# Kernel tuning notes

Measured on AMD Instinct MI355X. Metric: run time of the kernel, lower is better.

The kernel has to match this reference:

```python
import jax, jax.numpy as jnp
import numpy as np

WIN = (7, 7)
SHIFT = (3, 3)
HEADS = 8


def _rel_index():
    coords = np.stack(np.meshgrid(np.arange(WIN[0]), np.arange(WIN[1]), indexing='ij')).reshape(2, -1)
    rel = (coords[:, :, None] - coords[:, None, :]).transpose(1, 2, 0)  # [N,N,2]
    rel[:, :, 0] += WIN[0] - 1
    rel[:, :, 1] += WIN[1] - 1
    rel[:, :, 0] *= 2 * WIN[1] - 1
    return jnp.asarray(rel.sum(-1).reshape(-1).astype(np.int32))  # [N*N]


def _attn_mask(pad_H, pad_W):
    # standard Swin shifted-window mask (intended behavior of the source's mask block)
    img = np.zeros((pad_H, pad_W), np.float32)
    cnt = 0
    for h in ((0, -WIN[0]), (-WIN[0], -SHIFT[0]), (-SHIFT[0], None)):
        for w in ((0, -WIN[1]), (-WIN[1], -SHIFT[1]), (-SHIFT[1], None)):
            img[h[0]:h[1], w[0]:w[1]] = cnt
            cnt += 1
    nHw, nWw = pad_H // WIN[0], pad_W // WIN[1]
    m = img.reshape(nHw, WIN[0], nWw, WIN[1]).transpose(0, 2, 1, 3).reshape(nHw * nWw, WIN[0] * WIN[1])
    diff = m[:, None, :] - m[:, :, None]  # [nW, N, N]
    return jnp.asarray(np.where(diff != 0, -100.0, 0.0).astype(np.float32))


def setup_inputs() -> dict:
    key = jax.random.key(0)
    ks = jax.random.split(key, 6)
    B, H, W, C = 32, 56, 56, 256
    return {
        'x': jax.random.normal(ks[0], (B, H, W, C), jnp.float32),
        'qkv_weight': jax.random.normal(ks[1], (3 * C, C), jnp.float32) * (C ** -0.5),
        'qkv_bias': jnp.zeros((3 * C,), jnp.float32),
        'proj_weight': jax.random.normal(ks[2], (C, C), jnp.float32) * (C ** -0.5),
        'proj_bias': jnp.zeros((C,), jnp.float32),
        'rel_bias_table': jax.random.normal(ks[3], ((2 * WIN[0] - 1) * (2 * WIN[1] - 1), HEADS), jnp.float32) * 0.02,
        'rel_index': _rel_index(),
    }


def reference(x, qkv_weight, qkv_bias, proj_weight, proj_bias, rel_bias_table, rel_index):
    B, H, W, C = x.shape
    hd = C // HEADS
    N = WIN[0] * WIN[1]
    # relative position bias: [1, heads, N, N]
    bias = rel_bias_table[rel_index].reshape(N, N, HEADS).transpose(2, 0, 1)[None]
    # H, W chosen divisible by window -> pad is a no-op; cyclic shift
    xs = jnp.roll(x, (-SHIFT[0], -SHIFT[1]), axis=(1, 2))
    nHw, nWw = H // WIN[0], W // WIN[1]
    nW = nHw * nWw
    xw = xs.reshape(B, nHw, WIN[0], nWw, WIN[1], C).transpose(0, 1, 3, 2, 4, 5).reshape(B * nW, N, C)
    qkv = xw @ qkv_weight.T + qkv_bias                           # [B*nW, N, 3C]
    qkv = qkv.reshape(B * nW, N, 3, HEADS, hd).transpose(2, 0, 3, 1, 4)
    q, k, v = qkv[0] * hd ** -0.5, qkv[1], qkv[2]                # [B*nW, heads, N, hd]
    attn = jnp.einsum('whnd,whmd->whnm', q, k) + bias            # [B*nW, heads, N, N]
    mask = _attn_mask(H, W)                                      # [nW, N, N]
    attn = attn.reshape(B, nW, HEADS, N, N) + mask[None, :, None]
    attn = jax.nn.softmax(attn, axis=-1).reshape(B * nW, HEADS, N, N)
    out = jnp.einsum('whnm,whmd->wnhd', attn, v).reshape(B * nW, N, C)
    out = out @ proj_weight.T + proj_bias
    out = out.reshape(B, nHw, nWw, WIN[0], WIN[1], C).transpose(0, 1, 3, 2, 4, 5).reshape(B, H, W, C)
    out = jnp.roll(out, (SHIFT[0], SHIFT[1]), axis=(1, 2))
    return out
```

## Files before the change

### kernel.cpp

```cpp
#include <hip/hip_runtime.h>

typedef float f32x4 __attribute__((ext_vector_type(4)));
typedef __bf16 bf16x4 __attribute__((ext_vector_type(4)));
typedef __bf16 bf16x8 __attribute__((ext_vector_type(8)));
typedef short s16x4 __attribute__((ext_vector_type(4)));

#define DEVI static __device__ __forceinline__

DEVI f32x4 mfma_k32(bf16x8 a, bf16x8 b, f32x4 c) {
    return __builtin_amdgcn_mfma_f32_16x16x32_bf16(a, b, c, 0, 0, 0);
}

union B4 { bf16x4 h; s16x4 s; };
DEVI f32x4 mfma_k16(bf16x4 a, bf16x4 b, f32x4 c) {
    B4 ua, ub; ua.h = a; ub.h = b;
    return __builtin_amdgcn_mfma_f32_16x16x16bf16_1k(ua.s, ub.s, c, 0, 0, 0);
}

union F8 { bf16x8 v; bf16x4 h[2]; };

DEVI bf16x8 ld8_lds(const __bf16* p) {
    F8 f;
    f.h[0] = *(const bf16x4*)p;
    f.h[1] = *(const bf16x4*)(p + 4);
    return f.v;
}
DEVI bf16x8 ld8_gb(const __bf16* p) { return *(const bf16x8*)p; }
DEVI bf16x8 ldf8(const float* p) {
    f32x4 a = *(const f32x4*)p;
    f32x4 b = *(const f32x4*)(p + 4);
    F8 f;
#pragma unroll
    for (int j = 0; j < 4; ++j) {
        f.h[0][j] = (__bf16)a[j];
        f.h[1][j] = (__bf16)b[j];
    }
    return f.v;
}

__global__ __launch_bounds__(256) void k_w2bf(const float* __restrict__ wqkv,
                                              const float* __restrict__ wp,
                                              __bf16* __restrict__ o) {
    int i = blockIdx.x * 256 + threadIdx.x;
    int t = i >> 9, kc = (i >> 6) & 7, l = i & 63;
    int row = t * 16 + (l & 15);
    int col = kc * 32 + (l >> 4) * 8;
    const float* src = (t < 48) ? (wqkv + row * 256 + col)
                                : (wp + (row - 768) * 256 + col);
    f32x4 a = *(const f32x4*)src;
    f32x4 b = *(const f32x4*)(src + 4);
    F8 f;
#pragma unroll
    for (int j = 0; j < 4; ++j) { f.h[0][j] = (__bf16)a[j]; f.h[1][j] = (__bf16)b[j]; }
    *(bf16x8*)(o + (size_t)i * 8) = f.v;
}

__global__ __launch_bounds__(512)
__attribute__((amdgpu_waves_per_eu(4))) void k_swin(
    const float* __restrict__ x,
    const __bf16* __restrict__ wb,
    const float* __restrict__ bqkv,
    const float* __restrict__ btab,
    const float* __restrict__ pbias,
    float* __restrict__ out)
{
    __shared__ __align__(16) unsigned char smem[53936];
    __bf16* xw = (__bf16*)(smem);
    __bf16* cb = (__bf16*)(smem + 25480);
    __bf16* tb = (__bf16*)(smem + 50960);
    unsigned* tinfo = (unsigned*)(smem + 53680);

    const int tid = threadIdx.x;
    const int wid = tid >> 6, lane = tid & 63;
    const int li = lane & 15, g = lane >> 4;
    const int blk = blockIdx.x;
    const int b = blk >> 6, wi = blk & 63;
    const int wh = wi >> 3, ww = wi & 7;
    const int h = wid;

    for (int c = tid; c < 49 * 32; c += 512) {
        int tok = c >> 5, part = c & 31;
        int i = tok / 7, j = tok - 7 * i;
        int r = wh * 7 + i + 3;  if (r >= 56) r -= 56;
        int cc = ww * 7 + j + 3; if (cc >= 56) cc -= 56;
        F8 f; f.v = ldf8(x + (((size_t)(b * 56 + r) * 56 + cc) << 8) + (part << 3));
        __bf16* dst = xw + tok * 260 + (part << 3);
        *(bf16x4*)dst = f.h[0];
        *(bf16x4*)(dst + 4) = f.h[1];
    }
    for (int c = tid; c < 169 * 8; c += 512) {
        int idx = c >> 3, hh = c & 7;
        tb[hh * 170 + idx] = (__bf16)btab[c];
    }
    if (tid < 64) {
        int tok = tid;
        if (tok < 49) {
            int i = tok / 7, j = tok - 7 * i;
            unsigned rh = (wh == 7) ? (i < 4 ? 1u : 2u) : 0u;
            unsigned rw = (ww == 7) ? (j < 4 ? 1u : 2u) : 0u;
            tinfo[tok] = (unsigned)(13 * i + j) | ((rh * 3u + rw) << 16);
        } else {
            tinfo[tok] = 255u << 16;
        }
    }
    __syncthreads();

    const f32x4 zf = {0.f, 0.f, 0.f, 0.f};

    f32x4 qa[2][4], ka[2][4];
#pragma unroll
    for (int ct = 0; ct < 2; ++ct)
#pragma unroll
        for (int tt = 0; tt < 4; ++tt) { qa[ct][tt] = zf; ka[ct][tt] = zf; }

    const __bf16* wqb = wb + (size_t)(2 * h) * 4096 + lane * 8;
    const __bf16* wkb = wqb + 16 * 4096;
    const __bf16* wvb = wqb + 32 * 4096;

#pragma unroll
    for (int kc = 0; kc < 8; ++kc) {
        bf16x8 xf[4];
#pragma unroll
        for (int tt = 0; tt < 4; ++tt) {
            int row = 16 * tt + li; if (row > 48) row = 48;
            xf[tt] = ld8_lds(xw + row * 260 + kc * 32 + g * 8);
        }
#pragma unroll
        for (int ct = 0; ct < 2; ++ct) {
            bf16x8 aq = ld8_gb(wqb + ct * 4096 + kc * 512);
            bf16x8 ak = ld8_gb(wkb + ct * 4096 + kc * 512);
#pragma unroll
            for (int tt = 0; tt < 4; ++tt) {
                qa[ct][tt] = mfma_k32(aq, xf[tt], qa[ct][tt]);
                ka[ct][tt] = mfma_k32(ak, xf[tt], ka[ct][tt]);
            }
        }
    }

    bf16x4 qf[4][2], kf[4][2];
#pragma unroll
    for (int ct = 0; ct < 2; ++ct) {
        f32x4 bq = *(const f32x4*)(bqkv + h * 32 + 16 * ct + 4 * g);
        f32x4 bk = *(const f32x4*)(bqkv + 256 + h * 32 + 16 * ct + 4 * g);
#pragma unroll
        for (int tt = 0; tt < 4; ++tt)
#pragma unroll
            for (int r = 0; r < 4; ++r) {
                qf[tt][ct][r] = (__bf16)((qa[ct][tt][r] + bq[r]) * 0.17677669529663687f);
                kf[tt][ct][r] = (__bf16)(ka[ct][tt][r] + bk[r]);
            }
    }

    unsigned inMk[4][4];
#pragma unroll
    for (int kt = 0; kt < 4; ++kt)
#pragma unroll
        for (int r = 0; r < 4; ++r)
            inMk[kt][r] = tinfo[16 * kt + 4 * g + r];

    const __bf16* tbh = tb + h * 170 + 84;
    bf16x4 pf[4][4];
#pragma unroll
    for (int qt = 0; qt < 4; ++qt) {
        f32x4 sv[4];
#pragma unroll
        for (int kt = 0; kt < 4; ++kt) {
            f32x4 acc = zf;
            acc = mfma_k16(kf[kt][0], qf[qt][0], acc);
            acc = mfma_k16(kf[kt][1], qf[qt][1], acc);
            sv[kt] = acc;
        }
        unsigned inN = tinfo[16 * qt + li];
        int codeN = (int)(inN & 0xffffu);
        float mx = -1e30f;
#pragma unroll
        for (int kt = 0; kt < 4; ++kt)
#pragma unroll
            for (int r = 0; r < 4; ++r) {
                unsigned inM = inMk[kt][r];
                float v = sv[kt][r] + (float)tbh[codeN - (int)(inM & 0xffffu)]
                        + ((((inN ^ inM) >> 16) != 0u) ? -100.f : 0.f);
                if (kt == 3 && (r > 0 || g > 0)) v = -30000.f;
                sv[kt][r] = v;
                mx = fmaxf(mx, v);
            }
        mx = fmaxf(mx, __shfl_xor(mx, 16));
        mx = fmaxf(mx, __shfl_xor(mx, 32));
        float sum = 0.f;
#pragma unroll
        for (int kt = 0; kt < 4; ++kt)
#pragma unroll
            for (int r = 0; r < 4; ++r) {
                float e = __expf(sv[kt][r] - mx);
                sv[kt][r] = e;
                sum += e;
            }
        sum += __shfl_xor(sum, 16);
        sum += __shfl_xor(sum, 32);
        float inv = 1.0f / sum;
#pragma unroll
        for (int kt = 0; kt < 4; ++kt) {
            bf16x4 pp;
#pragma unroll
            for (int r = 0; r < 4; ++r) pp[r] = (__bf16)(sv[kt][r] * inv);
            pf[qt][kt] = pp;
        }
    }
    __builtin_amdgcn_sched_barrier(0);

    f32x4 va[4][2];
#pragma unroll
    for (int tt = 0; tt < 4; ++tt)
#pragma unroll
        for (int ct = 0; ct < 2; ++ct) va[tt][ct] = zf;
#pragma unroll
    for (int kc = 0; kc < 8; ++kc) {
        bf16x8 xf[4];
#pragma unroll
        for (int tt = 0; tt < 4; ++tt) {
            int row = 16 * tt + li; if (row > 48) row = 48;
            xf[tt] = ld8_lds(xw + row * 260 + kc * 32 + g * 8);
        }
#pragma unroll
        for (int ct = 0; ct < 2; ++ct) {
            bf16x8 bv = ld8_gb(wvb + ct * 4096 + kc * 512);
#pragma unroll
            for (int tt = 0; tt < 4; ++tt)
                va[tt][ct] = mfma_k32(xf[tt], bv, va[tt][ct]);
        }
    }
    bf16x4 vf[2][4];
#pragma unroll
    for (int ct = 0; ct < 2; ++ct) {
        float bv = bqkv[512 + h * 32 + 16 * ct + li];
#pragma unroll
        for (int tt = 0; tt < 4; ++tt)
#pragma unroll
            for (int r = 0; r < 4; ++r)
                vf[ct][tt][r] = (__bf16)(va[tt][ct][r] + bv);
    }

    f32x4 oa[4][2];
#pragma unroll
    for (int qt = 0; qt < 4; ++qt)
#pragma unroll
        for (int dt = 0; dt < 2; ++dt) {
            f32x4 acc = zf;
#pragma unroll
            for (int kt = 0; kt < 4; ++kt)
                acc = mfma_k16(pf[qt][kt], vf[dt][kt], acc);
            oa[qt][dt] = acc;
        }

#pragma unroll
    for (int qt = 0; qt < 4; ++qt)
#pragma unroll
        for (int r = 0; r < 4; ++r) {
            int q = 16 * qt + 4 * g + r;
            if (q < 49) {
#pragma unroll
                for (int dt = 0; dt < 2; ++dt)
                    cb[q * 260 + 32 * h + 16 * dt + li] = (__bf16)oa[qt][dt][r];
            }
        }
    __syncthreads();

    const int pm = wid >> 2, pn = wid & 3;
    f32x4 pacc[2][4];
#pragma unroll
    for (int mt = 0; mt < 2; ++mt)
#pragma unroll
        for (int nt = 0; nt < 4; ++nt) pacc[mt][nt] = zf;

    const __bf16* wpb = wb + (size_t)(48 + 4 * pn) * 4096 + lane * 8;
#pragma unroll
    for (int kc = 0; kc < 8; ++kc) {
        bf16x8 a[2];
#pragma unroll
        for (int mt = 0; mt < 2; ++mt) {
            int row = 32 * pm + 16 * mt + li; if (row > 48) row = 48;
            a[mt] = ld8_lds(cb + row * 260 + kc * 32 + g * 8);
        }
#pragma unroll
        for (int nt = 0; nt < 4; ++nt) {
            bf16x8 bb = ld8_gb(wpb + nt * 4096 + kc * 512);
#pragma unroll
            for (int mt = 0; mt < 2; ++mt)
                pacc[mt][nt] = mfma_k32(a[mt], bb, pacc[mt][nt]);
        }
    }

#pragma unroll
    for (int nt = 0; nt < 4; ++nt) {
        int o = 64 * pn + 16 * nt + li;
        float bias = pbias[o];
#pragma unroll
        for (int mt = 0; mt < 2; ++mt)
#pragma unroll
            for (int r = 0; r < 4; ++r) {
                int n = 32 * pm + 16 * mt + 4 * g + r;
                if (n < 49) {
                    int i = n / 7, j = n - 7 * i;
                    int rr = wh * 7 + i + 3; if (rr >= 56) rr -= 56;
                    int cc = ww * 7 + j + 3; if (cc >= 56) cc -= 56;
                    out[(((size_t)(b * 56 + rr) * 56 + cc) << 8) + o] =
                        pacc[mt][nt][r] + bias;
                }
            }
    }
}

extern "C" void kernel_launch(void* const* d_in, const int* in_sizes, int n_in,
                              void* d_out, int out_size, void* d_ws, size_t ws_size,
                              hipStream_t stream) {
    const float* x    = (const float*)d_in[0];
    const float* wqkv = (const float*)d_in[1];
    const float* bqkv = (const float*)d_in[2];
    const float* wp   = (const float*)d_in[3];
    const float* pb   = (const float*)d_in[4];
    const float* btab = (const float*)d_in[5];
    float* out = (float*)d_out;

    __bf16* wbuf = (__bf16*)d_ws;
    k_w2bf<<<128, 256, 0, stream>>>(wqkv, wp, wbuf);
    k_swin<<<2048, 512, 0, stream>>>(x, wbuf, bqkv, btab, pb, out);
}
```

Before: 287.9 us.

## Split Q/K projections and pack mask info to cut register pressure

Computes the Q and K projections in separate passes with scheduling barriers, so only one accumulator set is live at a time. The per-key token info is packed two per register, attention output is converted to bf16 right after the MFMA, and the launch bound changes from waves_per_eu(4) to a min-blocks hint of 6. The aim is fewer VGPRs and higher occupancy. The cost is reading the x tile from LDS an extra time and less interleaving of the Q and K MFMAs.

Result: slower. 364.5 us (+26.6%).

```diff
diff --git a/kernel.cpp b/kernel.cpp
--- a/kernel.cpp
+++ b/kernel.cpp
@@ -36,6 +36,12 @@
         f.h[1][j] = (__bf16)b[j];
     }
     return f.v;
+}
+DEVI bf16x4 pk4(f32x4 v) {
+    bf16x4 r;
+#pragma unroll
+    for (int j = 0; j < 4; ++j) r[j] = (__bf16)v[j];
+    return r;
 }
 
 __global__ __launch_bounds__(256) void k_w2bf(const float* __restrict__ wqkv,
@@ -55,8 +61,7 @@
     *(bf16x8*)(o + (size_t)i * 8) = f.v;
 }
 
-__global__ __launch_bounds__(512)
-__attribute__((amdgpu_waves_per_eu(4))) void k_swin(
+__global__ __launch_bounds__(512, 6) void k_swin(
     const float* __restrict__ x,
     const __bf16* __restrict__ wb,
     const float* __restrict__ bqkv,
@@ -98,65 +103,95 @@
             int i = tok / 7, j = tok - 7 * i;
             unsigned rh = (wh == 7) ? (i < 4 ? 1u : 2u) : 0u;
             unsigned rw = (ww == 7) ? (j < 4 ? 1u : 2u) : 0u;
-            tinfo[tok] = (unsigned)(13 * i + j) | ((rh * 3u + rw) << 16);
+            tinfo[tok] = (unsigned)(13 * i + j) | ((rh * 3u + rw) << 8);
         } else {
-            tinfo[tok] = 255u << 16;
+            tinfo[tok] = 255u << 8;
         }
     }
     __syncthreads();
 
     const f32x4 zf = {0.f, 0.f, 0.f, 0.f};
-
-    f32x4 qa[2][4], ka[2][4];
-#pragma unroll
-    for (int ct = 0; ct < 2; ++ct)
-#pragma unroll
-        for (int tt = 0; tt < 4; ++tt) { qa[ct][tt] = zf; ka[ct][tt] = zf; }
-
     const __bf16* wqb = wb + (size_t)(2 * h) * 4096 + lane * 8;
     const __bf16* wkb = wqb + 16 * 4096;
     const __bf16* wvb = wqb + 32 * 4096;
 
-#pragma unroll
-    for (int kc = 0; kc < 8; ++kc) {
-        bf16x8 xf[4];
-#pragma unroll
-        for (int tt = 0; tt < 4; ++tt) {
-            int row = 16 * tt + li; if (row > 48) row = 48;
-            xf[tt] = ld8_lds(xw + row * 260 + kc * 32 + g * 8);
+    bf16x4 qf[4][2], kf[4][2];
+
+    {
+        f32x4 acc[2][4];
+#pragma unroll
+        for (int ct = 0; ct < 2; ++ct)
+#pragma unroll
+            for (int tt = 0; tt < 4; ++tt) acc[ct][tt] = zf;
+#pragma unroll
+        for (int kc = 0; kc < 8; ++kc) {
+            bf16x8 xf[4];
+#pragma unroll
+            for (int tt = 0; tt < 4; ++tt) {
+                int row = 16 * tt + li; if (row > 48) row = 48;
+                xf[tt] = ld8_lds(xw + row * 260 + kc * 32 + g * 8);
+            }
+#pragma unroll
+            for (int ct = 0; ct < 2; ++ct) {
+                bf16x8 aq = ld8_gb(wqb + ct * 4096 + kc * 512);
+#pragma unroll
+                for (int tt = 0; tt < 4; ++tt)
+                    acc[ct][tt] = mfma_k32(aq, xf[tt], acc[ct][tt]);
+            }
         }
 #pragma unroll
         for (int ct = 0; ct < 2; ++ct) {
-            bf16x8 aq = ld8_gb(wqb + ct * 4096 + kc * 512);
-            bf16x8 ak = ld8_gb(wkb + ct * 4096 + kc * 512);
+            f32x4 bq = *(const f32x4*)(bqkv + h * 32 + 16 * ct + 4 * g);
+#pragma unroll
+            for (int tt = 0; tt < 4; ++tt)
+#pragma unroll
+                for (int r = 0; r < 4; ++r)
+                    qf[tt][ct][r] = (__bf16)((acc[ct][tt][r] + bq[r]) * 0.17677669529663687f);
+        }
+    }
+    __builtin_amdgcn_sched_barrier(0);
+
+    {
+        f32x4 acc[2][4];
+#pragma unroll
+        for (int ct = 0; ct < 2; ++ct)
+#pragma unroll
+            for (int tt = 0; tt < 4; ++tt) acc[ct][tt] = zf;
+#pragma unroll
+        for (int kc = 0; kc < 8; ++kc) {
+            bf16x8 xf[4];
 #pragma unroll
             for (int tt = 0; tt < 4; ++tt) {
-                qa[ct][tt] = mfma_k32(aq, xf[tt], qa[ct][tt]);
-                ka[ct][tt] = mfma_k32(ak, xf[tt], ka[ct][tt]);
-            }
-        }
-    }
-
-    bf16x4 qf[4][2], kf[4][2];
-#pragma unroll
-    for (int ct = 0; ct < 2; ++ct) {
-        f32x4 bq = *(const f32x4*)(bqkv + h * 32 + 16 * ct + 4 * g);
-        f32x4 bk = *(const f32x4*)(bqkv + 256 + h * 32 + 16 * ct + 4 * g);
-#pragma unroll
-        for (int tt = 0; tt < 4; ++tt)
-#pragma unroll
-            for (int r = 0; r < 4; ++r) {
-                qf[tt][ct][r] = (__bf16)((qa[ct][tt][r] + bq[r]) * 0.17677669529663687f);
-                kf[tt][ct][r] = (__bf16)(ka[ct][tt][r] + bk[r]);
-            }
-    }
-
-    unsigned inMk[4][4];
+                int row = 16 * tt + li; if (row > 48) row = 48;
+                xf[tt] = ld8_lds(xw + row * 260 + kc * 32 + g * 8);
+            }
+#pragma unroll
+            for (int ct = 0; ct < 2; ++ct) {
+                bf16x8 ak = ld8_gb(wkb + ct * 4096 + kc * 512);
+#pragma unroll
+                for (int tt = 0; tt < 4; ++tt)
+                    acc[ct][tt] = mfma_k32(ak, xf[tt], acc[ct][tt]);
+            }
+        }
+#pragma unroll
+        for (int ct = 0; ct < 2; ++ct) {
+            f32x4 bk = *(const f32x4*)(bqkv + 256 + h * 32 + 16 * ct + 4 * g);
+#pragma unroll
+            for (int tt = 0; tt < 4; ++tt)
+#pragma unroll
+                for (int r = 0; r < 4; ++r)
+                    kf[tt][ct][r] = (__bf16)(acc[ct][tt][r] + bk[r]);
+        }
+    }
+    __builtin_amdgcn_sched_barrier(0);
+
+    unsigned pkk[8];
 #pragma unroll
     for (int kt = 0; kt < 4; ++kt)
 #pragma unroll
-        for (int r = 0; r < 4; ++r)
-            inMk[kt][r] = tinfo[16 * kt + 4 * g + r];
+        for (int rp = 0; rp < 2; ++rp)
+            pkk[kt * 2 + rp] = tinfo[16 * kt + 4 * g + 2 * rp]
+                             | (tinfo[16 * kt + 4 * g + 2 * rp + 1] << 16);
 
     const __bf16* tbh = tb + h * 170 + 84;
     bf16x4 pf[4][4];
@@ -171,15 +206,15 @@
             sv[kt] = acc;
         }
         unsigned inN = tinfo[16 * qt + li];
-        int codeN = (int)(inN & 0xffffu);
+        int cN = (int)(inN & 255u);
         float mx = -1e30f;
 #pragma unroll
         for (int kt = 0; kt < 4; ++kt)
 #pragma unroll
             for (int r = 0; r < 4; ++r) {
-                unsigned inM = inMk[kt][r];
-                float v = sv[kt][r] + (float)tbh[codeN - (int)(inM & 0xffffu)]
-                        + ((((inN ^ inM) >> 16) != 0u) ? -100.f : 0.f);
+                unsigned m = (pkk[kt * 2 + (r >> 1)] >> (16 * (r & 1))) & 0xffffu;
+                float v = sv[kt][r] + (float)tbh[cN - (int)(m & 255u)]
+                        + ((((inN ^ m) & 0xff00u) != 0u) ? -100.f : 0.f);
                 if (kt == 3 && (r > 0 || g > 0)) v = -30000.f;
                 sv[kt][r] = v;
                 mx = fmaxf(mx, v);
@@ -208,39 +243,38 @@
     }
     __builtin_amdgcn_sched_barrier(0);
 
-    f32x4 va[4][2];
-#pragma unroll
-    for (int tt = 0; tt < 4; ++tt)
-#pragma unroll
-        for (int ct = 0; ct < 2; ++ct) va[tt][ct] = zf;
-#pragma unroll
-    for (int kc = 0; kc < 8; ++kc) {
-        bf16x8 xf[4];
-#pragma unroll
-        for (int tt = 0; tt < 4; ++tt) {
-            int row = 16 * tt + li; if (row > 48) row = 48;
-            xf[tt] = ld8_lds(xw + row * 260 + kc * 32 + g * 8);
+    bf16x4 vf[2][4];
+    {
+        f32x4 acc[4][2];
+#pragma unroll
+        for (int tt = 0; tt < 4; ++tt)
+#pragma unroll
+            for (int ct = 0; ct < 2; ++ct) acc[tt][ct] = zf;
+#pragma unroll
+        for (int kc = 0; kc < 8; ++kc) {
+            bf16x8 bv0 = ld8_gb(wvb + kc * 512);
+            bf16x8 bv1 = ld8_gb(wvb + 4096 + kc * 512);
+#pragma unroll
+            for (int tt = 0; tt < 4; ++tt) {
+                int row = 16 * tt + li; if (row > 48) row = 48;
+                bf16x8 xf = ld8_lds(xw + row * 260 + kc * 32 + g * 8);
+                acc[tt][0] = mfma_k32(xf, bv0, acc[tt][0]);
+                acc[tt][1] = mfma_k32(xf, bv1, acc[tt][1]);
+            }
         }
 #pragma unroll
         for (int ct = 0; ct < 2; ++ct) {
-            bf16x8 bv = ld8_gb(wvb + ct * 4096 + kc * 512);
+            float bv = bqkv[512 + h * 32 + 16 * ct + li];
 #pragma unroll
             for (int tt = 0; tt < 4; ++tt)
-                va[tt][ct] = mfma_k32(xf[tt], bv, va[tt][ct]);
-        }
-    }
-    bf16x4 vf[2][4];
-#pragma unroll
-    for (int ct = 0; ct < 2; ++ct) {
-        float bv = bqkv[512 + h * 32 + 16 * ct + li];
-#pragma unroll
-        for (int tt = 0; tt < 4; ++tt)
-#pragma unroll
-            for (int r = 0; r < 4; ++r)
-                vf[ct][tt][r] = (__bf16)(va[tt][ct][r] + bv);
-    }
-
-    f32x4 oa[4][2];
+#pragma unroll
+                for (int r = 0; r < 4; ++r)
+                    vf[ct][tt][r] = (__bf16)(acc[tt][ct][r] + bv);
+        }
+    }
+    __builtin_amdgcn_sched_barrier(0);
+
+    bf16x4 osv[4][2];
 #pragma unroll
     for (int qt = 0; qt < 4; ++qt)
 #pragma unroll
@@ -249,7 +283,7 @@
 #pragma unroll
             for (int kt = 0; kt < 4; ++kt)
                 acc = mfma_k16(pf[qt][kt], vf[dt][kt], acc);
-            oa[qt][dt] = acc;
+            osv[qt][dt] = pk4(acc);
         }
 
 #pragma unroll
@@ -260,7 +294,7 @@
             if (q < 49) {
 #pragma unroll
                 for (int dt = 0; dt < 2; ++dt)
-                    cb[q * 260 + 32 * h + 16 * dt + li] = (__bf16)oa[qt][dt][r];
+                    cb[q * 260 + 32 * h + 16 * dt + li] = osv[qt][dt][r];
             }
         }
     __syncthreads();
```

## Precompute combined relative-bias and shift-mask tables in MFMA fragment layout

Applied to the files above, without the earlier changes.

A prologue kernel now builds, for each of the four window boundary classes and each head, a float table holding relative position bias plus shift mask plus padding sentinel, laid out to match the MFMA accumulator fragments. The main kernel adds these with vector global loads instead of staging the bias table in LDS and doing per-element index arithmetic and mask comparisons. Output addresses are also precomputed per token into LDS rather than recomputed with divisions in the store loop. The cost is a 512 KB table read from global memory (likely L2-resident) on every score tile, in place of LDS lookups.

Measured after the change: 297.0 us. 1.03x slower.

```diff
diff --git a/kernel.cpp b/kernel.cpp
--- a/kernel.cpp
+++ b/kernel.cpp
@@ -38,21 +38,48 @@
     return f.v;
 }
 
-__global__ __launch_bounds__(256) void k_w2bf(const float* __restrict__ wqkv,
-                                              const float* __restrict__ wp,
-                                              __bf16* __restrict__ o) {
-    int i = blockIdx.x * 256 + threadIdx.x;
-    int t = i >> 9, kc = (i >> 6) & 7, l = i & 63;
-    int row = t * 16 + (l & 15);
-    int col = kc * 32 + (l >> 4) * 8;
-    const float* src = (t < 48) ? (wqkv + row * 256 + col)
-                                : (wp + (row - 768) * 256 + col);
-    f32x4 a = *(const f32x4*)src;
-    f32x4 b = *(const f32x4*)(src + 4);
-    F8 f;
-#pragma unroll
-    for (int j = 0; j < 4; ++j) { f.h[0][j] = (__bf16)a[j]; f.h[1][j] = (__bf16)b[j]; }
-    *(bf16x8*)(o + (size_t)i * 8) = f.v;
+__global__ __launch_bounds__(256) void k_pre(const float* __restrict__ wqkv,
+                                             const float* __restrict__ wp,
+                                             const float* __restrict__ btab,
+                                             __bf16* __restrict__ wout,
+                                             float* __restrict__ bmout) {
+    int bid = blockIdx.x;
+    if (bid < 128) {
+        int i = bid * 256 + threadIdx.x;
+        int t = i >> 9, kc = (i >> 6) & 7, l = i & 63;
+        int row = t * 16 + (l & 15);
+        int col = kc * 32 + (l >> 4) * 8;
+        const float* src = (t < 48) ? (wqkv + row * 256 + col)
+                                    : (wp + (row - 768) * 256 + col);
+        f32x4 a = *(const f32x4*)src;
+        f32x4 b = *(const f32x4*)(src + 4);
+        F8 f;
+#pragma unroll
+        for (int j = 0; j < 4; ++j) { f.h[0][j] = (__bf16)a[j]; f.h[1][j] = (__bf16)b[j]; }
+        *(bf16x8*)(wout + (size_t)i * 8) = f.v;
+    } else {
+        int i = (bid - 128) * 256 + threadIdx.x;
+        int r = i & 3, lane = (i >> 2) & 63;
+        int kt = (i >> 8) & 3, qt = (i >> 10) & 3, h = (i >> 12) & 7, cls = i >> 15;
+        int li = lane & 15, g = lane >> 4;
+        int q = 16 * qt + li;
+        int key = 16 * kt + 4 * g + r;
+        float v;
+        if (key >= 49) {
+            v = -30000.f;
+        } else if (q >= 49) {
+            v = 0.f;
+        } else {
+            int qi = q / 7, qj = q - 7 * qi;
+            int ki = key / 7, kj = key - 7 * ki;
+            float bias = btab[((qi - ki + 6) * 13 + (qj - kj + 6)) * 8 + h];
+            int ch = cls >> 1, cw = cls & 1;
+            int gq = (ch ? (qi < 4 ? 1 : 2) : 0) * 3 + (cw ? (qj < 4 ? 1 : 2) : 0);
+            int gk = (ch ? (ki < 4 ? 1 : 2) : 0) * 3 + (cw ? (kj < 4 ? 1 : 2) : 0);
+            v = bias + ((gq != gk) ? -100.f : 0.f);
+        }
+        bmout[i] = v;
+    }
 }
 
 __global__ __launch_bounds__(512)
@@ -60,15 +87,14 @@
     const float* __restrict__ x,
     const __bf16* __restrict__ wb,
     const float* __restrict__ bqkv,
-    const float* __restrict__ btab,
+    const float* __restrict__ bm,
     const float* __restrict__ pbias,
     float* __restrict__ out)
 {
-    __shared__ __align__(16) unsigned char smem[53936];
+    __shared__ __align__(16) unsigned char smem[51216];
     __bf16* xw = (__bf16*)(smem);
     __bf16* cb = (__bf16*)(smem + 25480);
-    __bf16* tb = (__bf16*)(smem + 50960);
-    unsigned* tinfo = (unsigned*)(smem + 53680);
+    unsigned* obase = (unsigned*)(smem + 50960);
 
     const int tid = threadIdx.x;
     const int wid = tid >> 6, lane = tid & 63;
@@ -77,6 +103,7 @@
     const int b = blk >> 6, wi = blk & 63;
     const int wh = wi >> 3, ww = wi & 7;
     const int h = wid;
+    const int cls = ((wh == 7) ? 2 : 0) + ((ww == 7) ? 1 : 0);
 
     for (int c = tid; c < 49 * 32; c += 512) {
         int tok = c >> 5, part = c & 31;
@@ -88,35 +115,25 @@
         *(bf16x4*)dst = f.h[0];
         *(bf16x4*)(dst + 4) = f.h[1];
     }
-    for (int c = tid; c < 169 * 8; c += 512) {
-        int idx = c >> 3, hh = c & 7;
-        tb[hh * 170 + idx] = (__bf16)btab[c];
-    }
-    if (tid < 64) {
-        int tok = tid;
-        if (tok < 49) {
-            int i = tok / 7, j = tok - 7 * i;
-            unsigned rh = (wh == 7) ? (i < 4 ? 1u : 2u) : 0u;
-            unsigned rw = (ww == 7) ? (j < 4 ? 1u : 2u) : 0u;
-            tinfo[tok] = (unsigned)(13 * i + j) | ((rh * 3u + rw) << 16);
-        } else {
-            tinfo[tok] = 255u << 16;
-        }
+    if (tid < 49) {
+        int i = tid / 7, j = tid - 7 * i;
+        int r = wh * 7 + i + 3;  if (r >= 56) r -= 56;
+        int cc = ww * 7 + j + 3; if (cc >= 56) cc -= 56;
+        obase[tid] = ((unsigned)((b * 56 + r) * 56 + cc)) << 8;
     }
     __syncthreads();
 
     const f32x4 zf = {0.f, 0.f, 0.f, 0.f};
-
-    f32x4 qa[2][4], ka[2][4];
-#pragma unroll
-    for (int ct = 0; ct < 2; ++ct)
-#pragma unroll
-        for (int tt = 0; tt < 4; ++tt) { qa[ct][tt] = zf; ka[ct][tt] = zf; }
-
     const __bf16* wqb = wb + (size_t)(2 * h) * 4096 + lane * 8;
     const __bf16* wkb = wqb + 16 * 4096;
     const __bf16* wvb = wqb + 32 * 4096;
 
+    f32x4 qa[2][4], ka[2][4];
+#pragma unroll
+    for (int ct = 0; ct < 2; ++ct)
+#pragma unroll
+        for (int tt = 0; tt < 4; ++tt) { qa[ct][tt] = zf; ka[ct][tt] = zf; }
+
 #pragma unroll
     for (int kc = 0; kc < 8; ++kc) {
         bf16x8 xf[4];
@@ -151,14 +168,7 @@
             }
     }
 
-    unsigned inMk[4][4];
-#pragma unroll
-    for (int kt = 0; kt < 4; ++kt)
-#pragma unroll
-        for (int r = 0; r < 4; ++r)
-            inMk[kt][r] = tinfo[16 * kt + 4 * g + r];
-
-    const __bf16* tbh = tb + h * 170 + 84;
+    const float* bmq = bm + cls * 32768 + h * 4096 + lane * 4;
     bf16x4 pf[4][4];
 #pragma unroll
     for (int qt = 0; qt < 4; ++qt) {
@@ -170,20 +180,14 @@
             acc = mfma_k16(kf[kt][1], qf[qt][1], acc);
             sv[kt] = acc;
         }
-        unsigned inN = tinfo[16 * qt + li];
-        int codeN = (int)(inN & 0xffffu);
+#pragma unroll
+        for (int kt = 0; kt < 4; ++kt)
+            sv[kt] += *(const f32x4*)(bmq + qt * 1024 + kt * 256);
         float mx = -1e30f;
 #pragma unroll
         for (int kt = 0; kt < 4; ++kt)
 #pragma unroll
-            for (int r = 0; r < 4; ++r) {
-                unsigned inM = inMk[kt][r];
-                float v = sv[kt][r] + (float)tbh[codeN - (int)(inM & 0xffffu)]
-                        + ((((inN ^ inM) >> 16) != 0u) ? -100.f : 0.f);
-                if (kt == 3 && (r > 0 || g > 0)) v = -30000.f;
-                sv[kt][r] = v;
-                mx = fmaxf(mx, v);
-            }
+            for (int r = 0; r < 4; ++r) mx = fmaxf(mx, sv[kt][r]);
         mx = fmaxf(mx, __shfl_xor(mx, 16));
         mx = fmaxf(mx, __shfl_xor(mx, 32));
         float sum = 0.f;
@@ -299,13 +303,8 @@
 #pragma unroll
             for (int r = 0; r < 4; ++r) {
                 int n = 32 * pm + 16 * mt + 4 * g + r;
-                if (n < 49) {
-                    int i = n / 7, j = n - 7 * i;
-                    int rr = wh * 7 + i + 3; if (rr >= 56) rr -= 56;
-                    int cc = ww * 7 + j + 3; if (cc >= 56) cc -= 56;
-                    out[(((size_t)(b * 56 + rr) * 56 + cc) << 8) + o] =
-                        pacc[mt][nt][r] + bias;
-                }
+                if (n < 49)
+                    out[obase[n] + (unsigned)o] = pacc[mt][nt][r] + bias;
             }
     }
 }
@@ -322,6 +321,7 @@
     float* out = (float*)d_out;
 
     __bf16* wbuf = (__bf16*)d_ws;
-    k_w2bf<<<128, 256, 0, stream>>>(wqkv, wp, wbuf);
-    k_swin<<<2048, 512, 0, stream>>>(x, wbuf, bqkv, btab, pb, out);
-}
+    float* bm = (float*)((char*)d_ws + 524288);
+    k_pre<<<640, 256, 0, stream>>>(wqkv, wp, btab, wbuf, bm);
+    k_swin<<<2048, 512, 0, stream>>>(x, wbuf, bqkv, bm, pb, out);
+}
```
